# Kernel tuning notes

Hardware: AMD Instinct MI355X
Metric: run time of the kernel (lower is better)

The kernel has to match this reference:

```python
import jax, jax.numpy as jnp
import numpy as np


def setup_inputs() -> dict:
    key = jax.random.key(0)
    k1, k2, k3 = jax.random.split(key, 3)
    b, c, h, w, S = 16, 512, 64, 64, 8
    x = jax.random.normal(k1, (b, c, h, w), dtype=jnp.float32)
    Wk = jax.random.normal(k2, (S, c), dtype=jnp.float32) * (1.0 / np.sqrt(c))  # mk.weight [S, c]
    Wv = jax.random.normal(k3, (c, S), dtype=jnp.float32) * (1.0 / np.sqrt(S))  # mv.weight [c, S]
    return {"x": x, "Wk": Wk, "Wv": Wv}


def reference(x, Wk, Wv):
    b, c, h, w = x.shape
    n = h * w
    q = x.reshape(b, c, n).transpose(0, 2, 1)          # [b, n, c]
    attn = jnp.einsum('bnc,sc->bns', q, Wk)            # mk: [b, n, S]
    attn = jax.nn.softmax(attn, axis=1)                # softmax over tokens (dim=1)
    attn = attn / (1e-9 + jnp.sum(attn, axis=2, keepdims=True))  # L1 renorm over S
    out = jnp.einsum('bns,cs->bnc', attn, Wv)          # mv: [b, n, c]
    out = out.transpose(0, 2, 1).reshape(b, c, h, w)
    return jax.nn.relu(x + out)
```

## Files before the change

kernel.cpp:

```cpp
#include <hip/hip_runtime.h>
#include <math.h>

#define BB 16
#define CC 512
#define NTOK 4096
#define SS 8
#define TT 128
#define NTILES (NTOK / TT)
#define RSTRIDE 36

typedef float nfloat4 __attribute__((ext_vector_type(4)));

__global__ __launch_bounds__(256) void k_logits(const float* __restrict__ x,
                                                const float* __restrict__ Wk,
                                                float* __restrict__ E,
                                                float* __restrict__ esum_p) {
    __shared__ float wkT[CC * SS];
    __shared__ float red[8 * 32 * RSTRIDE];
    __shared__ float esum[4 * SS];
    const int tid   = threadIdx.x;
    const int tn    = tid & 31;
    const int tc    = tid >> 5;
    const int blk   = blockIdx.x;
    const int b     = blk >> 5;
    const int ntile = blk & 31;
    const int n0    = ntile * TT + tn * 4;

    for (int k = tid; k < CC * SS; k += 256) {
        int s = k >> 9;
        int c = k & (CC - 1);
        wkT[c * SS + s] = Wk[k];
    }
    __syncthreads();

    float acc[4][SS];
#pragma unroll
    for (int i = 0; i < 4; ++i)
#pragma unroll
        for (int s = 0; s < SS; ++s) acc[i][s] = 0.f;

    const float* xb = x + (size_t)b * CC * NTOK + n0;
#pragma unroll 8
    for (int k = 0; k < CC / 8; ++k) {
        int c = tc + k * 8;
        float4 x4 = *(const float4*)(xb + (size_t)c * NTOK);
        const float* wk = &wkT[c * SS];
#pragma unroll
        for (int s = 0; s < SS; ++s) {
            float w = wk[s];
            acc[0][s] += x4.x * w;
            acc[1][s] += x4.y * w;
            acc[2][s] += x4.z * w;
            acc[3][s] += x4.w * w;
        }
    }

    float4* myred = (float4*)&red[tc * (32 * RSTRIDE) + tn * RSTRIDE];
#pragma unroll
    for (int i = 0; i < 4; ++i) {
        myred[i * 2]     = make_float4(acc[i][0], acc[i][1], acc[i][2], acc[i][3]);
        myred[i * 2 + 1] = make_float4(acc[i][4], acc[i][5], acc[i][6], acc[i][7]);
    }
    __syncthreads();

    float* outb = E + ((size_t)b * NTOK + (size_t)ntile * TT) * SS;
    float es = 0.f;
#pragma unroll
    for (int j = 0; j < 4; ++j) {
        int flat = tid + j * 256;
        int tnp  = flat >> 5;
        int rem  = flat & 31;
        float v = 0.f;
#pragma unroll
        for (int t = 0; t < 8; ++t) v += red[t * (32 * RSTRIDE) + tnp * RSTRIDE + rem];
        float e = __expf(v);
        outb[flat] = e;
        es += e;
    }
    es += __shfl_down(es, 8, 64);
    es += __shfl_down(es, 16, 64);
    es += __shfl_down(es, 32, 64);
    const int lane = tid & 63, wave = tid >> 6;
    if (lane < SS) esum[wave * SS + lane] = es;
    __syncthreads();
    if (tid < SS) {
        float t = esum[tid] + esum[SS + tid] + esum[2 * SS + tid] + esum[3 * SS + tid];
        esum_p[(b * NTILES + ntile) * SS + tid] = t;
    }
}

__global__ __launch_bounds__(256) void k_out(const float* __restrict__ x,
                                             const float* __restrict__ Wv,
                                             const float* __restrict__ E,
                                             const float* __restrict__ esum_p,
                                             float* __restrict__ out) {
    __shared__ float wv[CC * SS];
    __shared__ float ep[NTILES * SS];
    __shared__ float invl_s[SS];
    const int tid   = threadIdx.x;
    const int tn    = tid & 31;
    const int tc    = tid >> 5;
    const int blk   = blockIdx.x;
    const int b     = blk >> 6;
    const int rest  = blk & 63;
    const int ntile = rest >> 1;
    const int chalf = rest & 1;
    const int n0    = ntile * TT + tn * 4;

    ep[tid] = esum_p[b * (NTILES * SS) + tid];
    for (int k = tid; k < CC * SS; k += 256) wv[k] = Wv[k];
    __syncthreads();
    if (tid < SS) {
        float t = 0.f;
#pragma unroll
        for (int j = 0; j < NTILES; ++j) t += ep[j * SS + tid];
        invl_s[tid] = 1.0f / t;
    }
    __syncthreads();

    float invl[SS];
#pragma unroll
    for (int s = 0; s < SS; ++s) invl[s] = invl_s[s];

    const float* lg = E + ((size_t)b * NTOK + n0) * SS;
    float w[4][SS];
#pragma unroll
    for (int i = 0; i < 4; ++i) {
        float4 p0 = *(const float4*)(lg + i * 8);
        float4 p1 = *(const float4*)(lg + i * 8 + 4);
        float e[SS] = {p0.x, p0.y, p0.z, p0.w, p1.x, p1.y, p1.z, p1.w};
        float rs = 0.f;
#pragma unroll
        for (int s = 0; s < SS; ++s) {
            float p = e[s] * invl[s];
            w[i][s] = p;
            rs += p;
        }
        float inv = 1.0f / (1e-9f + rs);
#pragma unroll
        for (int s = 0; s < SS; ++s) w[i][s] *= inv;
    }

    const size_t xbase = (size_t)b * CC * NTOK + n0;
#pragma unroll 8
    for (int k = 0; k < CC / 16; ++k) {
        int c = chalf * (CC / 2) + tc + k * 8;
        const float* xp = x + xbase + (size_t)c * NTOK;
        float4 x4 = *(const float4*)xp;
        const float* wvc = &wv[c * SS];
        float o0 = 0.f, o1 = 0.f, o2 = 0.f, o3 = 0.f;
#pragma unroll
        for (int s = 0; s < SS; ++s) {
            float vv = wvc[s];
            o0 += w[0][s] * vv;
            o1 += w[1][s] * vv;
            o2 += w[2][s] * vv;
            o3 += w[3][s] * vv;
        }
        nfloat4 y;
        y.x = fmaxf(x4.x + o0, 0.f);
        y.y = fmaxf(x4.y + o1, 0.f);
        y.z = fmaxf(x4.z + o2, 0.f);
        y.w = fmaxf(x4.w + o3, 0.f);
        __builtin_nontemporal_store(y, (nfloat4*)(out + xbase + (size_t)c * NTOK));
    }
}

extern "C" void kernel_launch(void* const* d_in, const int* in_sizes, int n_in,
                              void* d_out, int out_size, void* d_ws, size_t ws_size,
                              hipStream_t stream) {
    const float* x  = (const float*)d_in[0];
    const float* Wk = (const float*)d_in[1];
    const float* Wv = (const float*)d_in[2];
    float* outp = (float*)d_out;

    float* E      = (float*)d_ws;
    float* esum_p = E + (size_t)BB * NTOK * SS;

    k_logits<<<BB * NTILES, 256, 0, stream>>>(x, Wk, E, esum_p);
    k_out<<<BB * NTILES * 2, 256, 0, stream>>>(x, Wv, E, esum_p, outp);
}
```

Measured before the change: 261.0 us.

## Fuse logits and output kernels via cooperative grid sync

Replaces the two-kernel pipeline with one cooperative kernel. Each block computes its exp logits tile, keeps it in shared memory, publishes partial sums, then waits on a grid-wide sync before normalising and writing the output. This removes the global round trip of the E buffer and a second kernel launch, and the x tile may still be in L2 when it is re-read. In exchange it relies on all 512 blocks being co-resident, halves the block count of the output phase, and adds a grid barrier; if the cooperative launch fails it falls back to the old two kernels.

Result: slower. 352.1 us (+34.9%).

```diff
diff --git a/kernel.cpp b/kernel.cpp
--- a/kernel.cpp
+++ b/kernel.cpp
@@ -1,5 +1,8 @@
 #include <hip/hip_runtime.h>
+#include <hip/hip_cooperative_groups.h>
 #include <math.h>
+
+namespace cg = cooperative_groups;
 
 #define BB 16
 #define CC 512
@@ -8,8 +11,148 @@
 #define TT 128
 #define NTILES (NTOK / TT)
 #define RSTRIDE 36
+#define ESTRIDE 136
 
 typedef float nfloat4 __attribute__((ext_vector_type(4)));
+
+__global__ __launch_bounds__(256) void k_fused(const float* __restrict__ x,
+                                               const float* __restrict__ Wk,
+                                               const float* __restrict__ Wv,
+                                               float* __restrict__ esum_p,
+                                               float* __restrict__ out) {
+    __shared__ float wbuf[CC * SS];
+    __shared__ float red[8 * 32 * RSTRIDE];
+    __shared__ __align__(16) float Es[SS * ESTRIDE];
+    __shared__ float esum[4 * SS];
+    __shared__ float invl_s[SS];
+
+    const int tid   = threadIdx.x;
+    const int tn    = tid & 31;
+    const int tc    = tid >> 5;
+    const int blk   = blockIdx.x;
+    const int b     = blk >> 5;
+    const int ntile = blk & 31;
+    const int n0    = ntile * TT + tn * 4;
+
+    for (int k = tid; k < CC * SS; k += 256) {
+        int s = k >> 9;
+        int c = k & (CC - 1);
+        wbuf[c * SS + s] = Wk[k];
+    }
+    __syncthreads();
+
+    float acc[4][SS];
+#pragma unroll
+    for (int i = 0; i < 4; ++i)
+#pragma unroll
+        for (int s = 0; s < SS; ++s) acc[i][s] = 0.f;
+
+    const float* xb = x + (size_t)b * CC * NTOK + n0;
+#pragma unroll 8
+    for (int k = 0; k < CC / 8; ++k) {
+        int c = tc + k * 8;
+        float4 x4 = *(const float4*)(xb + (size_t)c * NTOK);
+        const float* wk = &wbuf[c * SS];
+#pragma unroll
+        for (int s = 0; s < SS; ++s) {
+            float w = wk[s];
+            acc[0][s] += x4.x * w;
+            acc[1][s] += x4.y * w;
+            acc[2][s] += x4.z * w;
+            acc[3][s] += x4.w * w;
+        }
+    }
+
+    float4* myred = (float4*)&red[tc * (32 * RSTRIDE) + tn * RSTRIDE];
+#pragma unroll
+    for (int i = 0; i < 4; ++i) {
+        myred[i * 2]     = make_float4(acc[i][0], acc[i][1], acc[i][2], acc[i][3]);
+        myred[i * 2 + 1] = make_float4(acc[i][4], acc[i][5], acc[i][6], acc[i][7]);
+    }
+    __syncthreads();
+
+    float es = 0.f;
+#pragma unroll
+    for (int j = 0; j < 4; ++j) {
+        int flat = tid + j * 256;
+        int tnp  = flat >> 5;
+        int rem  = flat & 31;
+        float v = 0.f;
+#pragma unroll
+        for (int t = 0; t < 8; ++t) v += red[t * (32 * RSTRIDE) + tnp * RSTRIDE + rem];
+        float e = __expf(v);
+        Es[(tid & 7) * ESTRIDE + (flat >> 3)] = e;
+        es += e;
+    }
+    es += __shfl_down(es, 8, 64);
+    es += __shfl_down(es, 16, 64);
+    es += __shfl_down(es, 32, 64);
+    const int lane = tid & 63, wave = tid >> 6;
+    if (lane < SS) esum[wave * SS + lane] = es;
+    __syncthreads();
+    if (tid < SS) {
+        float t = esum[tid] + esum[SS + tid] + esum[2 * SS + tid] + esum[3 * SS + tid];
+        __hip_atomic_store(&esum_p[(b * NTILES + ntile) * SS + tid], t,
+                           __ATOMIC_RELEASE, __HIP_MEMORY_SCOPE_AGENT);
+    }
+    cg::this_grid().sync();
+
+    for (int k = tid; k < CC * SS; k += 256) wbuf[k] = Wv[k];
+    red[tid] = __hip_atomic_load(&esum_p[b * (NTILES * SS) + tid],
+                                 __ATOMIC_RELAXED, __HIP_MEMORY_SCOPE_AGENT);
+    __syncthreads();
+    if (tid < SS) {
+        float t = 0.f;
+#pragma unroll
+        for (int j = 0; j < NTILES; ++j) t += red[j * SS + tid];
+        invl_s[tid] = 1.0f / t;
+    }
+    __syncthreads();
+
+    float w[4][SS];
+#pragma unroll
+    for (int s = 0; s < SS; ++s) {
+        float iv = invl_s[s];
+        float4 ev = *(const float4*)&Es[s * ESTRIDE + tn * 4];
+        w[0][s] = ev.x * iv;
+        w[1][s] = ev.y * iv;
+        w[2][s] = ev.z * iv;
+        w[3][s] = ev.w * iv;
+    }
+#pragma unroll
+    for (int i = 0; i < 4; ++i) {
+        float rs = 0.f;
+#pragma unroll
+        for (int s = 0; s < SS; ++s) rs += w[i][s];
+        float inv = 1.0f / (1e-9f + rs);
+#pragma unroll
+        for (int s = 0; s < SS; ++s) w[i][s] *= inv;
+    }
+
+    const size_t xbase = (size_t)b * CC * NTOK + n0;
+#pragma unroll 8
+    for (int k = 0; k < CC / 8; ++k) {
+        int c = tc + k * 8;
+        const float* xp = x + xbase + (size_t)c * NTOK;
+        float4 x4 = *(const float4*)xp;
+        const float* wvc = &wbuf[c * SS];
+        float o0 = 0.f, o1 = 0.f, o2 = 0.f, o3 = 0.f;
+#pragma unroll
+        for (int s = 0; s < SS; ++s) {
+            float vv = wvc[s];
+            o0 += w[0][s] * vv;
+            o1 += w[1][s] * vv;
+            o2 += w[2][s] * vv;
+            o3 += w[3][s] * vv;
+        }
+        nfloat4 y;
+        y.x = fmaxf(x4.x + o0, 0.f);
+        y.y = fmaxf(x4.y + o1, 0.f);
+        y.z = fmaxf(x4.z + o2, 0.f);
+        y.w = fmaxf(x4.w + o3, 0.f);
+        __builtin_nontemporal_store(y, (nfloat4*)(out + xbase + (size_t)c * NTOK));
+    }
+}
 
 __global__ __launch_bounds__(256) void k_logits(const float* __restrict__ x,
                                                 const float* __restrict__ Wk,
@@ -174,9 +317,14 @@
     const float* Wv = (const float*)d_in[2];
     float* outp = (float*)d_out;
 
-    float* E      = (float*)d_ws;
-    float* esum_p = E + (size_t)BB * NTOK * SS;
-
-    k_logits<<<BB * NTILES, 256, 0, stream>>>(x, Wk, E, esum_p);
-    k_out<<<BB * NTILES * 2, 256, 0, stream>>>(x, Wv, E, esum_p, outp);
+    float* esum_p = (float*)d_ws;
+    float* E      = esum_p + (size_t)BB * NTILES * SS;
+
+    void* args[] = {(void*)&x, (void*)&Wk, (void*)&Wv, (void*)&esum_p, (void*)&outp};
+    hipError_t e = hipLaunchCooperativeKernel((void*)k_fused, dim3(BB * NTILES),
+                                              dim3(256), args, 0, stream);
+    if (e != hipSuccess) {
+        k_logits<<<BB * NTILES, 256, 0, stream>>>(x, Wk, E, esum_p);
+        k_out<<<BB * NTILES * 2, 256, 0, stream>>>(x, Wv, E, esum_p, outp);
+    }
 }
```
